# Performance work log

Measured on AMD Instinct MI355X. Metric: run time of the kernel, lower is better.

The kernel has to match this reference:

```python
import jax, jax.numpy as jnp
import numpy as np
import math

D = 1024
H = 16
DH = D // H
B, M, N = 4, 1024, 2048
LN_EPS = 1e-5


def setup_inputs() -> dict:
    key = jax.random.key(0)
    ks = jax.random.split(key, 8)
    s = 1.0 / math.sqrt(D)  # keep logits well-scaled
    return {
        "Q": jax.random.normal(ks[0], (B, M, D), jnp.float32),
        "KV": jax.random.normal(ks[1], (B, N, D), jnp.float32),
        "log_gate_bias": jax.random.normal(ks[2], (B, N), jnp.float32),
        "Wq": jax.random.normal(ks[3], (D, D), jnp.float32) * s,
        "bq": jnp.zeros((D,), jnp.float32),
        "Wk": jax.random.normal(ks[4], (D, D), jnp.float32) * s,
        "bk": jnp.zeros((D,), jnp.float32),
        "Wv": jax.random.normal(ks[5], (D, D), jnp.float32) * s,
        "bv": jnp.zeros((D,), jnp.float32),
        "Wo": jax.random.normal(ks[6], (D, D), jnp.float32) * s,
        "bo": jnp.zeros((D,), jnp.float32),
        "gamma": jnp.ones((D,), jnp.float32),
        "beta": jnp.zeros((D,), jnp.float32),
    }


def reference(Q, KV, log_gate_bias, Wq, bq, Wk, bk, Wv, bv, Wo, bo, gamma, beta):
    b, m, d = Q.shape
    n = KV.shape[1]
    # projections (torch Linear: x @ W.T + b), split heads -> (b, h, len, dh)
    q = (Q @ Wq.T + bq).reshape(b, m, H, DH).transpose(0, 2, 1, 3)
    k = (KV @ Wk.T + bk).reshape(b, n, H, DH).transpose(0, 2, 1, 3)
    v = (KV @ Wv.T + bv).reshape(b, n, H, DH).transpose(0, 2, 1, 3)
    scores = jnp.einsum('bhmd,bhnd->bhmn', q, k) / math.sqrt(DH)
    # additive gate bias broadcast over heads and queries: (b,1,1,n)
    scores = scores + log_gate_bias[:, None, None, :]
    attn = jax.nn.softmax(scores, axis=-1)
    out = jnp.einsum('bhmn,bhnd->bhmd', attn, v)
    out = out.transpose(0, 2, 1, 3).reshape(b, m, d)
    out = out @ Wo.T + bo
    # dropout p=0.0 (eval) -> identity; residual + LayerNorm
    x = Q + out
    mu = jnp.mean(x, axis=-1, keepdims=True)
    var = jnp.mean(jnp.square(x - mu), axis=-1, keepdims=True)
    return gamma * (x - mu) * jax.lax.rsqrt(var + LN_EPS) + beta
```

## Files before the change

kernel.cpp:

```cpp
#include <hip/hip_runtime.h>
#include <hip/hip_bf16.h>

#define DMODEL 1024
#define NHEAD  16
#define DHEAD  64
#define BB     4
#define MM     1024
#define NN     2048
#define LOG2E  1.4426950408889634f

typedef __attribute__((ext_vector_type(8))) short bf16x8;
typedef __attribute__((ext_vector_type(4))) float f32x4;

#define AS1 __attribute__((address_space(1)))
#define AS3 __attribute__((address_space(3)))

__device__ __forceinline__ unsigned short f2bf(float f) {
  unsigned int u = __builtin_bit_cast(unsigned int, f);
  unsigned int r = (u + 0x7fffu + ((u >> 16) & 1u)) >> 16;
  return (unsigned short)r;
}

__global__ __launch_bounds__(256)
void cast_all(const float* __restrict__ Q, const float* __restrict__ KV,
              const float* __restrict__ W0, const float* __restrict__ W1,
              const float* __restrict__ W2, const float* __restrict__ W3,
              unsigned short* __restrict__ oQ, unsigned short* __restrict__ oKV,
              unsigned short* __restrict__ o0, unsigned short* __restrict__ o1,
              unsigned short* __restrict__ o2, unsigned short* __restrict__ o3)
{
  const int bid = blockIdx.x;
  const float* s; unsigned short* d; int i;
  if (bid < 4096)       { s = Q;  d = oQ;  i = bid * 256 + threadIdx.x; }
  else if (bid < 12288) { s = KV; d = oKV; i = (bid - 4096) * 256 + threadIdx.x; }
  else {
    const int w = (bid - 12288) >> 10;
    s = w == 0 ? W0 : w == 1 ? W1 : w == 2 ? W2 : W3;
    d = w == 0 ? o0 : w == 1 ? o1 : w == 2 ? o2 : o3;
    i = ((bid - 12288) & 1023) * 256 + threadIdx.x;
  }
  const float4 v = ((const float4*)s)[i];
  union { unsigned short us[4]; unsigned long long u64; } o;
  o.us[0] = f2bf(v.x); o.us[1] = f2bf(v.y); o.us[2] = f2bf(v.z); o.us[3] = f2bf(v.w);
  *(unsigned long long*)(d + (size_t)i * 4) = o.u64;
}

__global__ __launch_bounds__(256)
void qkv_gemm(const unsigned short* __restrict__ Qbf,
              const unsigned short* __restrict__ KVbf,
              const unsigned short* __restrict__ Wqb,
              const unsigned short* __restrict__ Wkb,
              const unsigned short* __restrict__ Wvb,
              const float* __restrict__ bq, const float* __restrict__ bk,
              const float* __restrict__ bv,
              unsigned short* __restrict__ qout,
              unsigned short* __restrict__ kout,
              unsigned short* __restrict__ vtout)
{
  __shared__ unsigned short As[2][128 * 32];
  __shared__ unsigned short Ws[2][128 * 32];

  const int bid = blockIdx.x;
  const unsigned short* A; const unsigned short* W; const float* bias;
  int mode, lb, nmb;
  if (bid < 256)      { A = Qbf;  W = Wqb; bias = bq; mode = 0; lb = bid;       nmb = 4; }
  else if (bid < 768) { A = KVbf; W = Wkb; bias = bk; mode = 1; lb = bid - 256; nmb = 8; }
  else                { A = KVbf; W = Wvb; bias = bv; mode = 2; lb = bid - 768; nmb = 8; }
  const int xcd = lb & 7;
  const int l   = lb >> 3;
  const int mb  = xcd * nmb + (l >> 3);
  const int nb  = l & 7;

  const int tid  = threadIdx.x;
  const int wave = tid >> 6;
  const int lane = tid & 63;
  const int l15  = lane & 15;
  const int l4   = lane >> 4;
  const int wm   = wave >> 1;
  const int wn   = wave & 1;
  const size_t row0 = (size_t)mb * 128;
  const size_t col0 = (size_t)nb * 128;

  f32x4 acc[4][4] = {};

  const int cc0 = (wave * 2) * 64 + lane;
  const int cc1 = cc0 + 64;
  const int r0 = cc0 >> 2, sch0 = (cc0 & 3) ^ (r0 & 3);
  const int r1 = cc1 >> 2, sch1 = (cc1 & 3) ^ (r1 & 3);
  const unsigned short* ap0 = A + (row0 + r0) * DMODEL + sch0 * 8;
  const unsigned short* ap1 = A + (row0 + r1) * DMODEL + sch1 * 8;
  const unsigned short* wp0 = W + (col0 + r0) * DMODEL + sch0 * 8;
  const unsigned short* wp1 = W + (col0 + r1) * DMODEL + sch1 * 8;

  auto stage = [&](int buf) {
    __builtin_amdgcn_global_load_lds((const AS1 void*)ap0, (AS3 void*)(&As[buf][cc0 * 8]), 16, 0, 0);
    __builtin_amdgcn_global_load_lds((const AS1 void*)ap1, (AS3 void*)(&As[buf][cc1 * 8]), 16, 0, 0);
    __builtin_amdgcn_global_load_lds((const AS1 void*)wp0, (AS3 void*)(&Ws[buf][cc0 * 8]), 16, 0, 0);
    __builtin_amdgcn_global_load_lds((const AS1 void*)wp1, (AS3 void*)(&Ws[buf][cc1 * 8]), 16, 0, 0);
    ap0 += 32; ap1 += 32; wp0 += 32; wp1 += 32;
  };

  stage(0);

  for (int kt = 0; kt < 32; ++kt) {
    const int cur = kt & 1;
    if (kt < 31) {
      stage(cur ^ 1);
      asm volatile("s_waitcnt vmcnt(4)" ::: "memory");
    } else {
      asm volatile("s_waitcnt vmcnt(0)" ::: "memory");
    }
    __builtin_amdgcn_sched_barrier(0);
    __builtin_amdgcn_s_barrier();
    __builtin_amdgcn_sched_barrier(0);

    bf16x8 af[4], bfr[4];
#pragma unroll
    for (int mi = 0; mi < 4; ++mi) {
      int r = wm * 64 + mi * 16 + l15;
      af[mi] = *(const bf16x8*)&As[cur][r * 32 + ((l4 ^ (r & 3)) << 3)];
    }
#pragma unroll
    for (int ni = 0; ni < 4; ++ni) {
      int r = wn * 64 + ni * 16 + l15;
      bfr[ni] = *(const bf16x8*)&Ws[cur][r * 32 + ((l4 ^ (r & 3)) << 3)];
    }
    __builtin_amdgcn_s_setprio(1);
#pragma unroll
    for (int mi = 0; mi < 4; ++mi)
#pragma unroll
      for (int ni = 0; ni < 4; ++ni)
        acc[mi][ni] = __builtin_amdgcn_mfma_f32_16x16x32_bf16(af[mi], bfr[ni], acc[mi][ni], 0, 0, 0);
    __builtin_amdgcn_s_setprio(0);

    asm volatile("s_waitcnt lgkmcnt(0)" ::: "memory");
    __builtin_amdgcn_sched_barrier(0);
    __builtin_amdgcn_s_barrier();
    __builtin_amdgcn_sched_barrier(0);
  }

#pragma unroll
  for (int mi = 0; mi < 4; ++mi) {
#pragma unroll
    for (int ni = 0; ni < 4; ++ni) {
      const int col = (int)col0 + wn * 64 + ni * 16 + l15;
      const float bcol = bias[col];
      if (mode == 2) {
        const int row = (int)row0 + wm * 64 + mi * 16 + l4 * 4;
        const int b = row >> 11, n = row & 2047;
        const int h = col >> 6, d = col & 63;
        union { unsigned short us[4]; uint2 u; } pk;
#pragma unroll
        for (int i = 0; i < 4; ++i)
          pk.us[i] = __builtin_bit_cast(unsigned short, __float2bfloat16(acc[mi][ni][i] + bcol));
        *(uint2*)(vtout + (((size_t)(b * 16 + h) * 64 + d) << 11) + n) = pk.u;
      } else {
#pragma unroll
        for (int i = 0; i < 4; ++i) {
          const size_t row = row0 + wm * 64 + mi * 16 + l4 * 4 + i;
          float v = acc[mi][ni][i] + bcol;
          if (mode == 0) v *= (0.125f * LOG2E);
          (mode == 0 ? qout : kout)[row * DMODEL + col] =
            __builtin_bit_cast(unsigned short, __float2bfloat16(v));
        }
      }
    }
  }
}

__global__ __launch_bounds__(256)
void gemm_o(const unsigned short* __restrict__ A,
            const unsigned short* __restrict__ W,
            const float* __restrict__ bias,
            const float* __restrict__ resid,
            float* __restrict__ out)
{
  __shared__ unsigned short As[2][64 * 32];
  __shared__ unsigned short Ws[2][128 * 32];

  const int bid = blockIdx.x;
  const int xcd = bid & 7;
  const int l   = bid >> 3;
  const int mb  = xcd * 8 + (l >> 3);
  const int nb  = l & 7;

  const int tid  = threadIdx.x;
  const int wave = tid >> 6;
  const int lane = tid & 63;
  const int l15  = lane & 15;
  const int l4   = lane >> 4;
  const int wm   = wave >> 1;
  const int wn   = wave & 1;
  const size_t row0 = (size_t)mb * 64;
  const size_t col0 = (size_t)nb * 128;

  f32x4 acc[2][4] = {};

  const int ra = tid >> 2, scha = (tid & 3) ^ (ra & 3);
  const int cc0 = (wave * 2) * 64 + lane;
  const int cc1 = cc0 + 64;
  const int r0 = cc0 >> 2, sch0 = (cc0 & 3) ^ (r0 & 3);
  const int r1 = cc1 >> 2, sch1 = (cc1 & 3) ^ (r1 & 3);
  const unsigned short* ap  = A + (row0 + ra) * DMODEL + scha * 8;
  const unsigned short* wp0 = W + (col0 + r0) * DMODEL + sch0 * 8;
  const unsigned short* wp1 = W + (col0 + r1) * DMODEL + sch1 * 8;

  auto stage = [&](int buf) {
    __builtin_amdgcn_global_load_lds((const AS1 void*)ap,  (AS3 void*)(&As[buf][tid * 8]), 16, 0, 0);
    __builtin_amdgcn_global_load_lds((const AS1 void*)wp0, (AS3 void*)(&Ws[buf][cc0 * 8]), 16, 0, 0);
    __builtin_amdgcn_global_load_lds((const AS1 void*)wp1, (AS3 void*)(&Ws[buf][cc1 * 8]), 16, 0, 0);
    ap += 32; wp0 += 32; wp1 += 32;
  };

  stage(0);

  for (int kt = 0; kt < 32; ++kt) {
    const int cur = kt & 1;
    if (kt < 31) {
      stage(cur ^ 1);
      asm volatile("s_waitcnt vmcnt(3)" ::: "memory");
    } else {
      asm volatile("s_waitcnt vmcnt(0)" ::: "memory");
    }
    __builtin_amdgcn_sched_barrier(0);
    __builtin_amdgcn_s_barrier();
    __builtin_amdgcn_sched_barrier(0);

    bf16x8 af[2], bfr[4];
#pragma unroll
    for (int mi = 0; mi < 2; ++mi) {
      int r = wm * 32 + mi * 16 + l15;
      af[mi] = *(const bf16x8*)&As[cur][r * 32 + ((l4 ^ (r & 3)) << 3)];
    }
#pragma unroll
    for (int ni = 0; ni < 4; ++ni) {
      int r = wn * 64 + ni * 16 + l15;
      bfr[ni] = *(const bf16x8*)&Ws[cur][r * 32 + ((l4 ^ (r & 3)) << 3)];
    }
    __builtin_amdgcn_s_setprio(1);
#pragma unroll
    for (int mi = 0; mi < 2; ++mi)
#pragma unroll
      for (int ni = 0; ni < 4; ++ni)
        acc[mi][ni] = __builtin_amdgcn_mfma_f32_16x16x32_bf16(af[mi], bfr[ni], acc[mi][ni], 0, 0, 0);
    __builtin_amdgcn_s_setprio(0);

    asm volatile("s_waitcnt lgkmcnt(0)" ::: "memory");
    __builtin_amdgcn_sched_barrier(0);
    __builtin_amdgcn_s_barrier();
    __builtin_amdgcn_sched_barrier(0);
  }

#pragma unroll
  for (int mi = 0; mi < 2; ++mi) {
#pragma unroll
    for (int ni = 0; ni < 4; ++ni) {
      const int col = (int)col0 + wn * 64 + ni * 16 + l15;
      const float bcol = bias[col];
#pragma unroll
      for (int i = 0; i < 4; ++i) {
        const size_t row = row0 + wm * 32 + mi * 16 + l4 * 4 + i;
        const size_t idx = row * DMODEL + col;
        out[idx] = resid[idx] + acc[mi][ni][i] + bcol;
      }
    }
  }
}

__global__ __launch_bounds__(512, 4)
void attn_kernel(const unsigned short* __restrict__ qb,
                 const unsigned short* __restrict__ kb,
                 const unsigned short* __restrict__ vt,
                 const float* __restrict__ lgb,
                 unsigned short* __restrict__ attn)
{
  __shared__ unsigned short Ks[2][64 * 64];
  __shared__ unsigned short Vs[2][64 * 64];
  __shared__ float Gs[2][64];
  __shared__ unsigned short Ps[8][16 * 64];

  const int tid  = threadIdx.x;
  const int wave = tid >> 6;
  const int lane = tid & 63;
  const int l15  = lane & 15;
  const int l4   = lane >> 4;

  const int bid  = blockIdx.x;
  const int xcd  = bid & 7;
  const int slot = bid >> 3;
  const int m_i  = slot & 7;
  const int grp  = slot >> 3;
  const int bh   = grp * 8 + xcd;
  const int b    = bh >> 4;
  const int h    = bh & 15;
  const int m0   = m_i * 128;

  const unsigned short* qg = qb + ((size_t)(b * MM + m0)) * DMODEL + h * DHEAD;
  const unsigned short* kg = kb + ((size_t)b * NN) * DMODEL + h * DHEAD;
  const unsigned short* vg = vt + ((size_t)(b * NHEAD + h)) * (DHEAD * (size_t)NN);

  bf16x8 qf0, qf1;
  {
    const unsigned short* qrow = qg + (size_t)(wave * 16 + l15) * DMODEL;
    qf0 = *(const bf16x8*)(qrow + l4 * 8);
    qf1 = *(const bf16x8*)(qrow + 32 + l4 * 8);
  }

  bf16x8 ones;
  {
    const short one = (l15 == 0) ? (short)0x3f80 : (short)0;
#pragma unroll
    for (int j = 0; j < 8; ++j) ones[j] = one;
  }

  const int sr = tid >> 3;
  const int sc = (tid & 7) ^ (sr & 7);
  const unsigned short* kp = kg + (size_t)sr * DMODEL + (sc << 3);
  const unsigned short* vp = vg + (size_t)sr * NN + (sc << 3);
  const float* gp = lgb + (size_t)b * NN + lane;

  auto stage = [&](int buf) {
    if (wave == 0)
      __builtin_amdgcn_global_load_lds((const AS1 void*)gp, (AS3 void*)(&Gs[buf][lane]), 4, 0, 0);
    __builtin_amdgcn_global_load_lds((const AS1 void*)kp, (AS3 void*)(&Ks[buf][tid * 8]), 16, 0, 0);
    __builtin_amdgcn_global_load_lds((const AS1 void*)vp, (AS3 void*)(&Vs[buf][tid * 8]), 16, 0, 0);
    kp += 64 * DMODEL; vp += 64; gp += 64;
  };

  stage(0);

  f32x4 ovec[5] = {};
  float mrow = -1e30f;
  unsigned short* Pw = &Ps[wave][0];
  const int pbase = l15 * 128;
  const int s7 = l15 & 7;

  for (int nt = 0; nt < NN / 64; ++nt) {
    const int cur = nt & 1;
    asm volatile("s_waitcnt vmcnt(0)" ::: "memory");
    __builtin_amdgcn_sched_barrier(0);
    __builtin_amdgcn_s_barrier();
    __builtin_amdgcn_sched_barrier(0);
    if (nt < NN / 64 - 1) stage(cur ^ 1);

    f32x4 s[4];
    __builtin_amdgcn_s_setprio(1);
#pragma unroll
    for (int ni = 0; ni < 4; ++ni) {
      const int r = ni * 16 + l15;
      const int c0 = l4 ^ (r & 7);
      bf16x8 kf0 = *(const bf16x8*)&Ks[cur][r * 64 + (c0 << 3)];
      bf16x8 kf1 = *(const bf16x8*)&Ks[cur][r * 64 + ((c0 ^ 4) << 3)];
      f32x4 z = {};
      z = __builtin_amdgcn_mfma_f32_16x16x32_bf16(kf0, qf0, z, 0, 0, 0);
      s[ni] = __builtin_amdgcn_mfma_f32_16x16x32_bf16(kf1, qf1, z, 0, 0, 0);
    }
    __builtin_amdgcn_s_setprio(0);

    float tmax = -1e30f;
#pragma unroll
    for (int ni = 0; ni < 4; ++ni) {
      const float4 g = *(const float4*)&Gs[cur][ni * 16 + l4 * 4];
      s[ni][0] = fmaf(g.x, LOG2E, s[ni][0]);
      s[ni][1] = fmaf(g.y, LOG2E, s[ni][1]);
      s[ni][2] = fmaf(g.z, LOG2E, s[ni][2]);
      s[ni][3] = fmaf(g.w, LOG2E, s[ni][3]);
      tmax = fmaxf(tmax, fmaxf(fmaxf(s[ni][0], s[ni][1]), fmaxf(s[ni][2], s[ni][3])));
    }
    tmax = fmaxf(tmax, __shfl_xor(tmax, 16));
    tmax = fmaxf(tmax, __shfl_xor(tmax, 32));

    if (!__all(tmax <= mrow)) {
      const float mnew  = fmaxf(mrow, tmax);
      const float alpha = __builtin_amdgcn_exp2f(mrow - mnew);
      mrow = mnew;
      const int abase = l4 << 2;
#pragma unroll
      for (int i = 0; i < 4; ++i) {
        const float ai = __shfl(alpha, abase + i);
        ovec[0][i] *= ai; ovec[1][i] *= ai; ovec[2][i] *= ai;
        ovec[3][i] *= ai; ovec[4][i] *= ai;
      }
    }

#pragma unroll
    for (int ni = 0; ni < 4; ++ni) {
      union { unsigned short us[4]; uint2 u; } pk;
#pragma unroll
      for (int i = 0; i < 4; ++i)
        pk.us[i] = __builtin_bit_cast(unsigned short,
                     __float2bfloat16(__builtin_amdgcn_exp2f(s[ni][i] - mrow)));
      *(uint2*)((char*)Pw + pbase + (((ni * 4 + l4) ^ (s7 << 1)) << 3)) = pk.u;
    }
    asm volatile("s_waitcnt lgkmcnt(0)" ::: "memory");
    __builtin_amdgcn_sched_barrier(0);

    __builtin_amdgcn_s_setprio(1);
#pragma unroll
    for (int ks2 = 0; ks2 < 2; ++ks2) {
      const bf16x8 pf = *(const bf16x8*)((const char*)Pw + pbase + (((ks2 * 4 + l4) ^ s7) << 4));
#pragma unroll
      for (int di = 0; di < 4; ++di) {
        const int d = di * 16 + l15;
        const bf16x8 vf = *(const bf16x8*)&Vs[cur][d * 64 + (((ks2 * 4 + l4) ^ (d & 7)) << 3)];
        ovec[di] = __builtin_amdgcn_mfma_f32_16x16x32_bf16(pf, vf, ovec[di], 0, 0, 0);
      }
      ovec[4] = __builtin_amdgcn_mfma_f32_16x16x32_bf16(pf, ones, ovec[4], 0, 0, 0);
    }
    __builtin_amdgcn_s_setprio(0);
  }

  const int lsrc = lane & 48;
  float linv[4];
#pragma unroll
  for (int i = 0; i < 4; ++i)
    linv[i] = 1.0f / __shfl(ovec[4][i], lsrc);
#pragma unroll
  for (int di = 0; di < 4; ++di)
#pragma unroll
    for (int i = 0; i < 4; ++i) {
      const int row = m0 + wave * 16 + l4 * 4 + i;
      const int col = h * DHEAD + di * 16 + l15;
      attn[((size_t)(b * MM + row)) * DMODEL + col] =
        __builtin_bit_cast(unsigned short, __float2bfloat16(ovec[di][i] * linv[i]));
    }
}

__global__ __launch_bounds__(256)
void ln_kernel(const float* __restrict__ x, const float* __restrict__ gamma,
               const float* __restrict__ beta, float* __restrict__ out)
{
  __shared__ float sh1[4], sh2[4];
  const int t = threadIdx.x;
  const size_t row = blockIdx.x;
  const float4 v = ((const float4*)(x + row * DMODEL))[t];

  float s = v.x + v.y + v.z + v.w;
#pragma unroll
  for (int m = 1; m < 64; m <<= 1) s += __shfl_xor(s, m);
  if ((t & 63) == 0) sh1[t >> 6] = s;
  __syncthreads();
  const float mu = (sh1[0] + sh1[1] + sh1[2] + sh1[3]) * (1.0f / DMODEL);

  const float dx = v.x - mu, dy = v.y - mu, dz = v.z - mu, dw = v.w - mu;
  float q = dx * dx + dy * dy + dz * dz + dw * dw;
#pragma unroll
  for (int m = 1; m < 64; m <<= 1) q += __shfl_xor(q, m);
  if ((t & 63) == 0) sh2[t >> 6] = q;
  __syncthreads();
  const float var = (sh2[0] + sh2[1] + sh2[2] + sh2[3]) * (1.0f / DMODEL);
  const float rstd = rsqrtf(var + 1e-5f);

  const float4 g  = ((const float4*)gamma)[t];
  const float4 be = ((const float4*)beta)[t];
  float4 o;
  o.x = dx * rstd * g.x + be.x;
  o.y = dy * rstd * g.y + be.y;
  o.z = dz * rstd * g.z + be.z;
  o.w = dw * rstd * g.w + be.w;
  ((float4*)(out + row * DMODEL))[t] = o;
}

extern "C" void kernel_launch(void* const* d_in, const int* in_sizes, int n_in,
                              void* d_out, int out_size, void* d_ws, size_t ws_size,
                              hipStream_t stream)
{
  const float* Qf    = (const float*)d_in[0];
  const float* KVf   = (const float*)d_in[1];
  const float* lgb   = (const float*)d_in[2];
  const float* Wq    = (const float*)d_in[3];
  const float* bq    = (const float*)d_in[4];
  const float* Wk    = (const float*)d_in[5];
  const float* bk    = (const float*)d_in[6];
  const float* Wv    = (const float*)d_in[7];
  const float* bv    = (const float*)d_in[8];
  const float* Wo    = (const float*)d_in[9];
  const float* bo    = (const float*)d_in[10];
  const float* gamma = (const float*)d_in[11];
  const float* beta  = (const float*)d_in[12];
  float* out = (float*)d_out;

  char* ws = (char*)d_ws;
  unsigned short* Qbf   = (unsigned short*)(ws + 0);
  unsigned short* attnb = Qbf;
  unsigned short* KVbf  = (unsigned short*)(ws + 8388608);
  float*          xbuf  = (float*)(ws + 8388608);
  unsigned short* Wqb = (unsigned short*)(ws + 25165824);
  unsigned short* Wkb = (unsigned short*)(ws + 27262976);
  unsigned short* Wvb = (unsigned short*)(ws + 29360128);
  unsigned short* Wob = (unsigned short*)(ws + 31457280);
  unsigned short* qbuf  = (unsigned short*)(ws + 33554432);
  unsigned short* kbuf  = (unsigned short*)(ws + 41943040);
  unsigned short* vtbuf = (unsigned short*)(ws + 58720256);

  cast_all<<<16384, dim3(256), 0, stream>>>(Qf, KVf, Wq, Wk, Wv, Wo,
                                            Qbf, KVbf, Wqb, Wkb, Wvb, Wob);

  qkv_gemm<<<1280, dim3(256), 0, stream>>>(Qbf, KVbf, Wqb, Wkb, Wvb,
                                           bq, bk, bv, qbuf, kbuf, vtbuf);

  attn_kernel<<<512, dim3(512), 0, stream>>>(qbuf, kbuf, vtbuf, lgb, attnb);

  gemm_o<<<512, dim3(256), 0, stream>>>(attnb, Wob, bo, Qf, xbuf);

  ln_kernel<<<4096, dim3(256), 0, stream>>>(xbuf, gamma, beta, out);
}
```

Before: 169.5 us.

## Process two key tiles per iteration with four-deep K/V LDS buffering

Restructures the attention main loop to handle 128 keys per iteration as two 64-key sub-tiles. K and V get four LDS buffers so the next pair of tiles loads while the current pair is computed. The gate bias is now read straight from global memory into registers instead of being staged through LDS. This halves the number of loop-top waits and barriers per key and lets both QK^T sub-tiles issue back to back. In exchange, LDS use roughly doubles, which can cut the number of resident blocks per CU, and an extra barrier is added at the end of each iteration.

```diff
diff --git a/kernel.cpp b/kernel.cpp
--- a/kernel.cpp
+++ b/kernel.cpp
@@ -267,6 +267,60 @@
   }
 }
 
+__device__ __forceinline__ void smpv(f32x4 (&s)[4], const f32x4 (&g)[4],
+                                     const unsigned short* Vsb, unsigned short* Pw,
+                                     f32x4 (&ovec)[5], float& mrow, const bf16x8& ones,
+                                     int l4, int pbase, int s7)
+{
+  float tmax = -1e30f;
+#pragma unroll
+  for (int ni = 0; ni < 4; ++ni) {
+#pragma unroll
+    for (int i = 0; i < 4; ++i)
+      s[ni][i] = fmaf(g[ni][i], LOG2E, s[ni][i]);
+    tmax = fmaxf(tmax, fmaxf(fmaxf(s[ni][0], s[ni][1]), fmaxf(s[ni][2], s[ni][3])));
+  }
+  tmax = fmaxf(tmax, __shfl_xor(tmax, 16));
+  tmax = fmaxf(tmax, __shfl_xor(tmax, 32));
+
+  if (!__all(tmax <= mrow)) {
+    const float mnew  = fmaxf(mrow, tmax);
+    const float alpha = __builtin_amdgcn_exp2f(mrow - mnew);
+    mrow = mnew;
+    const int abase = l4 << 2;
+#pragma unroll
+    for (int i = 0; i < 4; ++i) {
+      const float ai = __shfl(alpha, abase + i);
+      ovec[0][i] *= ai; ovec[1][i] *= ai; ovec[2][i] *= ai;
+      ovec[3][i] *= ai; ovec[4][i] *= ai;
+    }
+  }
+
+#pragma unroll
+  for (int ni = 0; ni < 4; ++ni) {
+    union { unsigned short us[4]; uint2 u; } pk;
+#pragma unroll
+    for (int i = 0; i < 4; ++i)
+      pk.us[i] = __builtin_bit_cast(unsigned short,
+                   __float2bfloat16(__builtin_amdgcn_exp2f(s[ni][i] - mrow)));
+    *(uint2*)((char*)Pw + pbase + (((ni * 4 + l4) ^ (s7 << 1)) << 3)) = pk.u;
+  }
+
+  __builtin_amdgcn_s_setprio(1);
+#pragma unroll
+  for (int ks2 = 0; ks2 < 2; ++ks2) {
+    const bf16x8 pf = *(const bf16x8*)((const char*)Pw + pbase + (((ks2 * 4 + l4) ^ s7) << 4));
+#pragma unroll
+    for (int di = 0; di < 4; ++di) {
+      const int d = di * 16 + (pbase >> 7);
+      const bf16x8 vf = *(const bf16x8*)&Vsb[d * 64 + (((ks2 * 4 + l4) ^ (d & 7)) << 3)];
+      ovec[di] = __builtin_amdgcn_mfma_f32_16x16x32_bf16(pf, vf, ovec[di], 0, 0, 0);
+    }
+    ovec[4] = __builtin_amdgcn_mfma_f32_16x16x32_bf16(pf, ones, ovec[4], 0, 0, 0);
+  }
+  __builtin_amdgcn_s_setprio(0);
+}
+
 __global__ __launch_bounds__(512, 4)
 void attn_kernel(const unsigned short* __restrict__ qb,
                  const unsigned short* __restrict__ kb,
@@ -274,9 +328,8 @@
                  const float* __restrict__ lgb,
                  unsigned short* __restrict__ attn)
 {
-  __shared__ unsigned short Ks[2][64 * 64];
-  __shared__ unsigned short Vs[2][64 * 64];
-  __shared__ float Gs[2][64];
+  __shared__ unsigned short Ks[4][64 * 64];
+  __shared__ unsigned short Vs[4][64 * 64];
   __shared__ unsigned short Ps[8][16 * 64];
 
   const int tid  = threadIdx.x;
@@ -298,6 +351,7 @@
   const unsigned short* qg = qb + ((size_t)(b * MM + m0)) * DMODEL + h * DHEAD;
   const unsigned short* kg = kb + ((size_t)b * NN) * DMODEL + h * DHEAD;
   const unsigned short* vg = vt + ((size_t)(b * NHEAD + h)) * (DHEAD * (size_t)NN);
+  const float* gg = lgb + (size_t)b * NN;
 
   bf16x8 qf0, qf1;
   {
@@ -317,17 +371,15 @@
   const int sc = (tid & 7) ^ (sr & 7);
   const unsigned short* kp = kg + (size_t)sr * DMODEL + (sc << 3);
   const unsigned short* vp = vg + (size_t)sr * NN + (sc << 3);
-  const float* gp = lgb + (size_t)b * NN + lane;
-
-  auto stage = [&](int buf) {
-    if (wave == 0)
-      __builtin_amdgcn_global_load_lds((const AS1 void*)gp, (AS3 void*)(&Gs[buf][lane]), 4, 0, 0);
+
+  auto stageT = [&](int buf) {
     __builtin_amdgcn_global_load_lds((const AS1 void*)kp, (AS3 void*)(&Ks[buf][tid * 8]), 16, 0, 0);
     __builtin_amdgcn_global_load_lds((const AS1 void*)vp, (AS3 void*)(&Vs[buf][tid * 8]), 16, 0, 0);
-    kp += 64 * DMODEL; vp += 64; gp += 64;
+    kp += 64 * DMODEL; vp += 64;
   };
 
-  stage(0);
+  stageT(0);
+  stageT(1);
 
   f32x4 ovec[5] = {};
   float mrow = -1e30f;
@@ -335,79 +387,59 @@
   const int pbase = l15 * 128;
   const int s7 = l15 & 7;
 
-  for (int nt = 0; nt < NN / 64; ++nt) {
-    const int cur = nt & 1;
+  for (int p = 0; p < 16; ++p) {
+    const int c0 = (p & 1) * 2;
+    const int c1 = c0 + 1;
+
     asm volatile("s_waitcnt vmcnt(0)" ::: "memory");
     __builtin_amdgcn_sched_barrier(0);
     __builtin_amdgcn_s_barrier();
     __builtin_amdgcn_sched_barrier(0);
-    if (nt < NN / 64 - 1) stage(cur ^ 1);
-
-    f32x4 s[4];
+
+    f32x4 g0[4], g1[4];
+    const float* gb = gg + p * 128 + l4 * 4;
+#pragma unroll
+    for (int ni = 0; ni < 4; ++ni) {
+      g0[ni] = *(const f32x4*)(gb + ni * 16);
+      g1[ni] = *(const f32x4*)(gb + 64 + ni * 16);
+    }
+
+    f32x4 s0[4], s1[4];
     __builtin_amdgcn_s_setprio(1);
 #pragma unroll
     for (int ni = 0; ni < 4; ++ni) {
       const int r = ni * 16 + l15;
-      const int c0 = l4 ^ (r & 7);
-      bf16x8 kf0 = *(const bf16x8*)&Ks[cur][r * 64 + (c0 << 3)];
-      bf16x8 kf1 = *(const bf16x8*)&Ks[cur][r * 64 + ((c0 ^ 4) << 3)];
+      const int cch = l4 ^ (r & 7);
+      bf16x8 kf0 = *(const bf16x8*)&Ks[c0][r * 64 + (cch << 3)];
+      bf16x8 kf1 = *(const bf16x8*)&Ks[c0][r * 64 + ((cch ^ 4) << 3)];
       f32x4 z = {};
       z = __builtin_amdgcn_mfma_f32_16x16x32_bf16(kf0, qf0, z, 0, 0, 0);
-      s[ni] = __builtin_amdgcn_mfma_f32_16x16x32_bf16(kf1, qf1, z, 0, 0, 0);
+      s0[ni] = __builtin_amdgcn_mfma_f32_16x16x32_bf16(kf1, qf1, z, 0, 0, 0);
+    }
+#pragma unroll
+    for (int ni = 0; ni < 4; ++ni) {
+      const int r = ni * 16 + l15;
+      const int cch = l4 ^ (r & 7);
+      bf16x8 kf0 = *(const bf16x8*)&Ks[c1][r * 64 + (cch << 3)];
+      bf16x8 kf1 = *(const bf16x8*)&Ks[c1][r * 64 + ((cch ^ 4) << 3)];
+      f32x4 z = {};
+      z = __builtin_amdgcn_mfma_f32_16x16x32_bf16(kf0, qf0, z, 0, 0, 0);
+      s1[ni] = __builtin_amdgcn_mfma_f32_16x16x32_bf16(kf1, qf1, z, 0, 0, 0);
     }
     __builtin_amdgcn_s_setprio(0);
 
-    float tmax = -1e30f;
-#pragma unroll
-    for (int ni = 0; ni < 4; ++ni) {
-      const float4 g = *(const float4*)&Gs[cur][ni * 16 + l4 * 4];
-      s[ni][0] = fmaf(g.x, LOG2E, s[ni][0]);
-      s[ni][1] = fmaf(g.y, LOG2E, s[ni][1]);
-      s[ni][2] = fmaf(g.z, LOG2E, s[ni][2]);
-      s[ni][3] = fmaf(g.w, LOG2E, s[ni][3]);
-      tmax = fmaxf(tmax, fmaxf(fmaxf(s[ni][0], s[ni][1]), fmaxf(s[ni][2], s[ni][3])));
-    }
-    tmax = fmaxf(tmax, __shfl_xor(tmax, 16));
-    tmax = fmaxf(tmax, __shfl_xor(tmax, 32));
-
-    if (!__all(tmax <= mrow)) {
-      const float mnew  = fmaxf(mrow, tmax);
-      const float alpha = __builtin_amdgcn_exp2f(mrow - mnew);
-      mrow = mnew;
-      const int abase = l4 << 2;
-#pragma unroll
-      for (int i = 0; i < 4; ++i) {
-        const float ai = __shfl(alpha, abase + i);
-        ovec[0][i] *= ai; ovec[1][i] *= ai; ovec[2][i] *= ai;
-        ovec[3][i] *= ai; ovec[4][i] *= ai;
-      }
-    }
-
-#pragma unroll
-    for (int ni = 0; ni < 4; ++ni) {
-      union { unsigned short us[4]; uint2 u; } pk;
-#pragma unroll
-      for (int i = 0; i < 4; ++i)
-        pk.us[i] = __builtin_bit_cast(unsigned short,
-                     __float2bfloat16(__builtin_amdgcn_exp2f(s[ni][i] - mrow)));
-      *(uint2*)((char*)Pw + pbase + (((ni * 4 + l4) ^ (s7 << 1)) << 3)) = pk.u;
-    }
+    if (p < 15) {
+      stageT(c0 ^ 2);
+      stageT(c1 ^ 2);
+    }
+
+    smpv(s0, g0, &Vs[c0][0], Pw, ovec, mrow, ones, l4, pbase, s7);
+    smpv(s1, g1, &Vs[c1][0], Pw, ovec, mrow, ones, l4, pbase, s7);
+
     asm volatile("s_waitcnt lgkmcnt(0)" ::: "memory");
     __builtin_amdgcn_sched_barrier(0);
-
-    __builtin_amdgcn_s_setprio(1);
-#pragma unroll
-    for (int ks2 = 0; ks2 < 2; ++ks2) {
-      const bf16x8 pf = *(const bf16x8*)((const char*)Pw + pbase + (((ks2 * 4 + l4) ^ s7) << 4));
-#pragma unroll
-      for (int di = 0; di < 4; ++di) {
-        const int d = di * 16 + l15;
-        const bf16x8 vf = *(const bf16x8*)&Vs[cur][d * 64 + (((ks2 * 4 + l4) ^ (d & 7)) << 3)];
-        ovec[di] = __builtin_amdgcn_mfma_f32_16x16x32_bf16(pf, vf, ovec[di], 0, 0, 0);
-      }
-      ovec[4] = __builtin_amdgcn_mfma_f32_16x16x32_bf16(pf, ones, ovec[4], 0, 0, 0);
-    }
-    __builtin_amdgcn_s_setprio(0);
+    __builtin_amdgcn_s_barrier();
+    __builtin_amdgcn_sched_barrier(0);
   }
 
   const int lsrc = lane & 48;
```

Result: slower. 173.5 us (+2.4%).
